# Optimization experiments

Measured on AMD Instinct MI355X. Metric: run time of the kernel, lower is better.

## Reference

```python
import jax, jax.numpy as jnp
import numpy as np

N = 50000   # nodes
E = 600000  # edges (avg degree 12)
D = 128     # node_feat_size == graph_feat_size


def setup_inputs() -> dict:
    key = jax.random.key(0)
    ks = jax.random.split(key, 10)
    return {
        "node_feats": jax.random.normal(ks[0], (N, D), jnp.float32),
        "src": jax.random.randint(ks[1], (E,), 0, N),
        "dst": jax.random.randint(ks[2], (E,), 0, N),
        # project_edge: Linear(2D, 1)
        "W_edge": jax.random.normal(ks[3], (2 * D, 1), jnp.float32) * 0.05,
        "b_edge": jnp.zeros((1,), jnp.float32),
        # project_node: Linear(D, D)
        "W_proj": jax.random.normal(ks[4], (D, D), jnp.float32) * 0.05,
        "b_proj": jnp.zeros((D,), jnp.float32),
        # GRUCell(input=D, hidden=D)
        "W_ih": jax.random.normal(ks[5], (3 * D, D), jnp.float32) * 0.05,
        "W_hh": jax.random.normal(ks[6], (3 * D, D), jnp.float32) * 0.05,
        "b_ih": jnp.zeros((3 * D,), jnp.float32),
        "b_hh": jnp.zeros((3 * D,), jnp.float32),
        # BatchNorm1d(D) affine params (training-mode batch stats)
        "bn_gamma": jnp.ones((D,), jnp.float32),
        "bn_beta": jnp.zeros((D,), jnp.float32),
    }


def reference(node_feats, src, dst, W_edge, b_edge, W_proj, b_proj,
              W_ih, W_hh, b_ih, b_hh, bn_gamma, bn_beta):
    n_nodes = node_feats.shape[0]
    # apply_edges: he = concat([dst_feats, src_feats])  -> [E, 2D]
    he = jnp.concatenate([node_feats[dst], node_feats[src]], axis=1)
    # project_edge: Linear(2D,1) + LeakyReLU(0.01) -> edge logits [E]
    logits = jax.nn.leaky_relu(he @ W_edge + b_edge, 0.01)[:, 0]
    # DGL edge_softmax: softmax over incoming edges of each dst node
    mx = jax.ops.segment_max(logits, dst, num_segments=n_nodes)
    ex = jnp.exp(logits - mx[dst])
    denom = jax.ops.segment_sum(ex, dst, num_segments=n_nodes)
    a = ex / denom[dst]
    e = a + 1.0  # g.edata['e'] = a + 1
    # project_node (dropout is identity in eval) -> hv [N, D]
    hv = node_feats @ W_proj + b_proj
    # src_mul_edge + sum aggregation: c[v] = sum_{(u->v)} hv[u] * e
    msg = hv[src] * e[:, None]                       # [E, D]
    c = jax.ops.segment_sum(msg, dst, num_segments=n_nodes)
    context = jax.nn.elu(c)
    # GRUCell(context, node_feats)
    gi = context @ W_ih.T + b_ih
    gh = node_feats @ W_hh.T + b_hh
    i_r, i_z, i_n = jnp.split(gi, 3, axis=1)
    h_r, h_z, h_n = jnp.split(gh, 3, axis=1)
    r = jax.nn.sigmoid(i_r + h_r)
    z = jax.nn.sigmoid(i_z + h_z)
    n = jnp.tanh(i_n + r * h_n)
    h = (1.0 - z) * n + z * node_feats
    out = jax.nn.relu(h)
    # BatchNorm1d (training-mode batch statistics, eps=1e-5)
    mean = out.mean(axis=0)
    var = out.var(axis=0)
    return (out - mean) / jnp.sqrt(var + 1e-5) * bn_gamma + bn_beta
```

## Files before the change

kernel.cpp:

```cpp
#include <hip/hip_runtime.h>
#include <math.h>

constexpr int D = 128;
constexpr int BCAP = 4096;

typedef __attribute__((ext_vector_type(8))) short short8;
typedef __attribute__((ext_vector_type(4))) float f32x4;
typedef unsigned short ushort_t;
typedef unsigned int uint_t;

__device__ inline ushort_t f2b(float x) {
    uint_t u = __float_as_uint(x);
    uint_t r = u + 0x7fffu + ((u >> 16) & 1u);
    return (ushort_t)(r >> 16);
}
__device__ inline float b2f(ushort_t b) { return __uint_as_float(((uint_t)b) << 16); }

__device__ inline float sigm(float x) { return 1.f / (1.f + __expf(-x)); }
__device__ inline float tanh_(float x) {
    float t = __expf(-2.f * fabsf(x));
    float y = (1.f - t) / (1.f + t);
    return x >= 0.f ? y : -y;
}

__global__ __launch_bounds__(256) void k_prep_w(
    const float* __restrict__ W_ih, const float* __restrict__ W_hh,
    const float* __restrict__ W_proj,
    ushort_t* __restrict__ Wih16, ushort_t* __restrict__ Whh16,
    ushort_t* __restrict__ WpT16,
    int* __restrict__ gcur, float* __restrict__ bn8, int NBK)
{
    int idx = blockIdx.x * 256 + threadIdx.x;
    if (idx < 49152) {
        Wih16[idx] = f2b(W_ih[idx]);
    } else if (idx < 98304) {
        int i = idx - 49152;
        Whh16[i] = f2b(W_hh[i]);
    } else if (idx < 114688) {
        int t = idx - 98304;
        int j = t >> 7, k = t & 127;
        WpT16[t] = f2b(W_proj[k * 128 + j]);
    } else if (idx < 114688 + 256) {
        int t = idx - 114688;
        if (t < NBK) gcur[t] = t * BCAP;
    } else if (idx < 114688 + 256 + 2048) {
        bn8[idx - 114688 - 256] = 0.f;
    }
}

constexpr int EPT = 16;
__global__ __launch_bounds__(256, 2) void k_hv_part(
    const float* __restrict__ nf, const ushort_t* __restrict__ WpT16,
    const float* __restrict__ b_proj, const float* __restrict__ W_edge,
    ushort_t* __restrict__ nf16, ushort_t* __restrict__ hv16,
    float* __restrict__ s_d, float* __restrict__ s_s,
    const int* __restrict__ src, const int* __restrict__ dst,
    int* __restrict__ gcur, uint_t* __restrict__ pre_rec,
    int N, int NBK, int E, int nb_part)
{
    __shared__ ushort_t plds[16384];

    if ((int)blockIdx.x < nb_part) {
        int* cnt   = (int*)plds;
        int* gbase = cnt + 256;
        int tid = threadIdx.x;
        int base = blockIdx.x * (256 * EPT);
        for (int i = tid; i < NBK; i += 256) cnt[i] = 0;
        __syncthreads();
        uint_t rec[EPT], pw[EPT];
#pragma unroll
        for (int i = 0; i < EPT; ++i) {
            int e = base + i * 256 + tid;
            uint_t r = 0, p = 0xFFFFFFFFu;
            if (e < E) {
                int s = src[e], t = dst[e];
                int b = t >> 8;
                int old = atomicAdd(&cnt[b], 1);
                r = (uint_t)s | ((uint_t)(t & 255) << 16);
                p = ((uint_t)b << 16) | (uint_t)old;
            }
            rec[i] = r; pw[i] = p;
        }
        __syncthreads();
        for (int bkt = tid; bkt < NBK; bkt += 256) {
            int c = cnt[bkt];
            gbase[bkt] = c ? atomicAdd(&gcur[bkt], c) : 0;
        }
        __syncthreads();
#pragma unroll
        for (int i = 0; i < EPT; ++i) {
            if (pw[i] != 0xFFFFFFFFu) {
                int b = pw[i] >> 16;
                int old = pw[i] & 0xFFFF;
                pre_rec[gbase[b] + old] = rec[i];
            }
        }
        return;
    }

    int bid = blockIdx.x - nb_part;
    int w = threadIdx.x >> 6, lane = threadIdx.x & 63;
    int am = lane & 15, hi = lane >> 4, ak = hi * 8;

#pragma unroll
    for (int i = 0; i < 8; ++i) {
        int dl = (w * 8 + i) * 4 + hi;
        short8 v = *(const short8*)(WpT16 + (size_t)dl * 128 + am * 8);
        *(short8*)(plds + dl * 128 + ((am ^ (dl & 15)) * 8)) = v;
    }

    int r0 = bid * 64 + w * 16;
    int arow = r0 + am;
    bool aok = arow < N;
    short8 A[4];
    float pd = 0.f, ps = 0.f;
#pragma unroll
    for (int kf = 0; kf < 4; ++kf) {
        int ko = kf * 32 + ak;
        float4 f0 = {0,0,0,0}, f1 = {0,0,0,0};
        if (aok) {
            f0 = *(const float4*)(nf + (size_t)arow * 128 + ko);
            f1 = *(const float4*)(nf + (size_t)arow * 128 + ko + 4);
        }
        pd += f0.x * W_edge[ko]     + f0.y * W_edge[ko + 1]
            + f0.z * W_edge[ko + 2] + f0.w * W_edge[ko + 3]
            + f1.x * W_edge[ko + 4] + f1.y * W_edge[ko + 5]
            + f1.z * W_edge[ko + 6] + f1.w * W_edge[ko + 7];
        ps += f0.x * W_edge[128+ko]     + f0.y * W_edge[128+ko+1]
            + f0.z * W_edge[128+ko+2]   + f0.w * W_edge[128+ko+3]
            + f1.x * W_edge[128+ko+4]   + f1.y * W_edge[128+ko+5]
            + f1.z * W_edge[128+ko+6]   + f1.w * W_edge[128+ko+7];
        short8 a;
        a[0] = (short)f2b(f0.x); a[1] = (short)f2b(f0.y);
        a[2] = (short)f2b(f0.z); a[3] = (short)f2b(f0.w);
        a[4] = (short)f2b(f1.x); a[5] = (short)f2b(f1.y);
        a[6] = (short)f2b(f1.z); a[7] = (short)f2b(f1.w);
        A[kf] = a;
        if (aok) *(short8*)(nf16 + (size_t)arow * 128 + ko) = a;
    }
    pd += __shfl_xor(pd, 16); pd += __shfl_xor(pd, 32);
    ps += __shfl_xor(ps, 16); ps += __shfl_xor(ps, 32);
    if (hi == 0 && aok) { s_d[arow] = pd; s_s[arow] = ps; }

    __syncthreads();

    int crow0 = r0 + hi * 4;
#pragma unroll 2
    for (int nc = 0; nc < 8; ++nc) {
        f32x4 acc = {0.f, 0.f, 0.f, 0.f};
        int col = nc * 16 + am;
#pragma unroll
        for (int kf = 0; kf < 4; ++kf) {
            short8 B = *(const short8*)(plds + col * 128 + (((kf * 4 + hi) ^ am) * 8));
            acc = __builtin_amdgcn_mfma_f32_16x16x32_bf16(A[kf], B, acc, 0, 0, 0);
        }
        float b = b_proj[col];
#pragma unroll
        for (int r = 0; r < 4; ++r) {
            int grow = crow0 + r;
            if (grow < N) hv16[(size_t)grow * 128 + col] = f2b(acc[r] + b);
        }
    }
}

__global__ __launch_bounds__(256) void k_bucket(
    const uint_t* __restrict__ pre_rec, const int* __restrict__ gcur,
    const float* __restrict__ s_d, const float* __restrict__ s_s,
    const float* __restrict__ b_edge,
    int* __restrict__ row_start, int* __restrict__ row_cnt,
    uint2* __restrict__ edge_rec, float* __restrict__ den, int N)
{
    __shared__ int cnt[256], offx[256], cur[256], sdata[256];
    __shared__ float sdl[256], denl[256];
    int b = blockIdx.x, tid = threadIdx.x;
    int node = (b << 8) + tid;
    cnt[tid] = 0; cur[tid] = 0; denl[tid] = 0.f;
    sdl[tid] = (node < N) ? s_d[node] : 0.f;
    __syncthreads();
    int rs0 = b * BCAP, rs1 = gcur[b];
    for (int i = rs0 + tid; i < rs1; i += 256)
        atomicAdd(&cnt[(pre_rec[i] >> 16) & 255], 1);
    __syncthreads();
    int v = cnt[tid];
    int incl = v;
    sdata[tid] = incl; __syncthreads();
#pragma unroll
    for (int off = 1; off < 256; off <<= 1) {
        int add = (tid >= off) ? sdata[tid - off] : 0;
        __syncthreads();
        incl += add;
        sdata[tid] = incl;
        __syncthreads();
    }
    offx[tid] = incl - v;
    if (node < N) {
        row_start[node] = rs0 + incl - v;
        row_cnt[node] = v;
    }
    __syncthreads();
    float bias = b_edge[0];
    for (int i = rs0 + tid; i < rs1; i += 256) {
        uint_t rec = pre_rec[i];
        int sidx = rec & 0xFFFF;
        int dl = (rec >> 16) & 255;
        float l = sdl[dl] + s_s[sidx] + bias;
        l = l > 0.f ? l : 0.01f * l;
        float ev = __expf(l);
        int lp = atomicAdd(&cur[dl], 1);
        uint2 r;
        r.x = (uint_t)sidx;
        r.y = __float_as_uint(ev);
        edge_rec[rs0 + offx[dl] + lp] = r;
        atomicAdd(&denl[dl], ev);
    }
    __syncthreads();
    if (node < N) den[node] = denl[tid];
}

__global__ __launch_bounds__(256) void k_agg4(
    const ushort_t* __restrict__ hv16, const int* __restrict__ row_start,
    const int* __restrict__ row_cnt, const float* __restrict__ den,
    const uint2* __restrict__ edge_rec, ushort_t* __restrict__ ctx16, int N)
{
    __shared__ uint2 elds[8][128];
    int w = threadIdx.x >> 6, lane = threadIdx.x & 63;
    int half = lane >> 5;
    int hl = lane & 31;
    int nid = w * 2 + half;
    int v = blockIdx.x * 8 + nid;
    bool vok = v < N;

    int beg = 0, cnt = 0;
    float dv = 0.f;
    if (vok) {
        beg = row_start[v];
        cnt = row_cnt[v];
        dv = den[v];
        int cap0 = min(cnt, 128);
        for (int c = hl; c < cap0; c += 32)
            elds[nid][c] = edge_rec[beg + c];
    }
    float inv = dv > 0.f ? 1.f / dv : 0.f;

    float c0 = 0.f, c1 = 0.f, c2 = 0.f, c3 = 0.f;
    int cap = min(cnt, 128);
    for (int t0 = 0; t0 < cap; t0 += 8) {
        uint2 p[8];
        float wt[8];
#pragma unroll
        for (int k = 0; k < 8; ++k) {
            int tt = t0 + k;
            uint2 er = elds[nid][tt < cap ? tt : 0];
            wt[k] = (tt < cap) ? fmaf(__uint_as_float(er.y), inv, 1.0f) : 0.f;
            p[k] = ((const uint2*)(hv16 + ((size_t)er.x << 7)))[hl];
        }
#pragma unroll
        for (int k = 0; k < 8; ++k) {
            c0 = fmaf(b2f((ushort_t)p[k].x), wt[k], c0);
            c1 = fmaf(b2f((ushort_t)(p[k].x >> 16)), wt[k], c1);
            c2 = fmaf(b2f((ushort_t)p[k].y), wt[k], c2);
            c3 = fmaf(b2f((ushort_t)(p[k].y >> 16)), wt[k], c3);
        }
    }
    for (int c = 128; c < cnt; ++c) {
        uint2 er = edge_rec[beg + c];
        float wt2 = fmaf(__uint_as_float(er.y), inv, 1.0f);
        uint2 p2 = ((const uint2*)(hv16 + ((size_t)er.x << 7)))[hl];
        c0 = fmaf(b2f((ushort_t)p2.x), wt2, c0);
        c1 = fmaf(b2f((ushort_t)(p2.x >> 16)), wt2, c1);
        c2 = fmaf(b2f((ushort_t)p2.y), wt2, c2);
        c3 = fmaf(b2f((ushort_t)(p2.y >> 16)), wt2, c3);
    }
    if (!vok) return;
    c0 = c0 > 0.f ? c0 : expm1f(c0);
    c1 = c1 > 0.f ? c1 : expm1f(c1);
    c2 = c2 > 0.f ? c2 : expm1f(c2);
    c3 = c3 > 0.f ? c3 : expm1f(c3);
    uint2 outp;
    outp.x = (uint_t)f2b(c0) | ((uint_t)f2b(c1) << 16);
    outp.y = (uint_t)f2b(c2) | ((uint_t)f2b(c3) << 16);
    ((uint2*)ctx16)[(size_t)v * 32 + hl] = outp;
}

__global__ __launch_bounds__(1024, 1) void k_gru_mfma(
    const ushort_t* __restrict__ ctx16, const ushort_t* __restrict__ nf16,
    const ushort_t* __restrict__ Wih16, const ushort_t* __restrict__ Whh16,
    const float* __restrict__ b_ih, const float* __restrict__ b_hh,
    float* __restrict__ out, float* __restrict__ bn8, int N)
{
    __shared__ ushort_t wlds[6 * 8192];
    __shared__ float bnsum[2][16][64];
    int tid = threadIdx.x;
    int w = tid >> 6, lane = tid & 63;
    int am = lane & 15, hi = lane >> 4, ak = hi * 8;
    int g64 = blockIdx.y * 64;

    for (int q = tid; q < 6144; q += 1024) {
        int m = q >> 10;
        int rem = q & 1023;
        int col = rem >> 4;
        int kc = rem & 15;
        const ushort_t* sb = (m & 1) ? Whh16 : Wih16;
        short8 v = *(const short8*)(sb + (size_t)((m >> 1) * 128 + g64 + col) * 128 + kc * 8);
        *(short8*)(wlds + m * 8192 + col * 128 + ((kc ^ (col & 15)) * 8)) = v;
    }
    __syncthreads();

    float br_[4], bz_[4], bi_[4], bh_[4];
#pragma unroll
    for (int cf = 0; cf < 4; ++cf) {
        int dgl = g64 + cf * 16 + am;
        br_[cf] = b_ih[dgl] + b_hh[dgl];
        bz_[cf] = b_ih[128 + dgl] + b_hh[128 + dgl];
        bi_[cf] = b_ih[256 + dgl];
        bh_[cf] = b_hh[256 + dgl];
    }
    float cs[4] = {0,0,0,0}, cs2[4] = {0,0,0,0};

    for (int r0 = blockIdx.x * 256; r0 < N; r0 += gridDim.x * 256) {
        int rbase = r0 + w * 16;
        int arow = rbase + am;
        bool aok = arow < N;
        short8 z8 = {0,0,0,0,0,0,0,0};
        short8 Ac[4], An[4];
#pragma unroll
        for (int kf = 0; kf < 4; ++kf) {
            size_t off = (size_t)arow * 128 + kf * 32 + ak;
            Ac[kf] = aok ? *(const short8*)(ctx16 + off) : z8;
            An[kf] = aok ? *(const short8*)(nf16 + off) : z8;
        }
        int crow0 = rbase + hi * 4;
#pragma unroll 1
        for (int cf = 0; cf < 4; ++cf) {
            int dgl = g64 + cf * 16 + am;
            float hp_pre[4];
#pragma unroll
            for (int r = 0; r < 4; ++r) {
                int grow = crow0 + r;
                hp_pre[r] = (grow < N) ? b2f(nf16[(size_t)grow * 128 + dgl]) : 0.f;
            }
            f32x4 racc = {0,0,0,0}, zacc = {0,0,0,0};
            f32x4 iacc = {0,0,0,0}, hacc = {0,0,0,0};
#pragma unroll
            for (int kf = 0; kf < 4; ++kf) {
                const ushort_t* bp = wlds + (cf * 16 + am) * 128
                                   + ((((kf << 2) + hi) ^ am) * 8);
                short8 Br = *(const short8*)(bp + 0 * 8192);
                short8 Cr = *(const short8*)(bp + 1 * 8192);
                short8 Bz = *(const short8*)(bp + 2 * 8192);
                short8 Cz = *(const short8*)(bp + 3 * 8192);
                short8 Bi = *(const short8*)(bp + 4 * 8192);
                short8 Ch = *(const short8*)(bp + 5 * 8192);
                racc = __builtin_amdgcn_mfma_f32_16x16x32_bf16(Ac[kf], Br, racc, 0, 0, 0);
                racc = __builtin_amdgcn_mfma_f32_16x16x32_bf16(An[kf], Cr, racc, 0, 0, 0);
                zacc = __builtin_amdgcn_mfma_f32_16x16x32_bf16(Ac[kf], Bz, zacc, 0, 0, 0);
                zacc = __builtin_amdgcn_mfma_f32_16x16x32_bf16(An[kf], Cz, zacc, 0, 0, 0);
                iacc = __builtin_amdgcn_mfma_f32_16x16x32_bf16(Ac[kf], Bi, iacc, 0, 0, 0);
                hacc = __builtin_amdgcn_mfma_f32_16x16x32_bf16(An[kf], Ch, hacc, 0, 0, 0);
            }
#pragma unroll
            for (int r = 0; r < 4; ++r) {
                int grow = crow0 + r;
                float rv = sigm(racc[r] + br_[cf]);
                float zv = sigm(zacc[r] + bz_[cf]);
                float nv = tanh_(iacc[r] + bi_[cf] + rv * (hacc[r] + bh_[cf]));
                float h = (1.f - zv) * nv + zv * hp_pre[r];
                h = fmaxf(h, 0.f);
                if (grow < N) out[(size_t)grow * 128 + dgl] = h;
                else h = 0.f;
                cs[cf] += h;
                cs2[cf] = fmaf(h, h, cs2[cf]);
            }
        }
    }

#pragma unroll
    for (int cf = 0; cf < 4; ++cf) {
        cs[cf]  += __shfl_xor(cs[cf], 16);  cs[cf]  += __shfl_xor(cs[cf], 32);
        cs2[cf] += __shfl_xor(cs2[cf], 16); cs2[cf] += __shfl_xor(cs2[cf], 32);
        if (hi == 0) {
            bnsum[0][w][cf * 16 + am] = cs[cf];
            bnsum[1][w][cf * 16 + am] = cs2[cf];
        }
    }
    __syncthreads();
    int bin = (blockIdx.x & 7) * 256;
    if (tid < 64) {
        float s = 0.f;
#pragma unroll
        for (int wv = 0; wv < 16; ++wv) s += bnsum[0][wv][tid];
        atomicAdd(&bn8[bin + g64 + tid], s);
    } else if (tid < 128) {
        int c2 = tid - 64;
        float s2 = 0.f;
#pragma unroll
        for (int wv = 0; wv < 16; ++wv) s2 += bnsum[1][wv][c2];
        atomicAdd(&bn8[bin + 128 + g64 + c2], s2);
    }
}

__global__ __launch_bounds__(256) void k_bnnorm(
    float* __restrict__ out, const float* __restrict__ bn8,
    const float* __restrict__ gamma, const float* __restrict__ beta, int N)
{
    __shared__ float a_s[128], c_s[128];
    int tid = threadIdx.x;
    if (tid < 128) {
        float s = 0.f, s2 = 0.f;
#pragma unroll
        for (int b = 0; b < 8; ++b) {
            s  += bn8[b * 256 + tid];
            s2 += bn8[b * 256 + 128 + tid];
        }
        float invN = 1.f / (float)N;
        float mean = s * invN;
        float var = s2 * invN - mean * mean;
        float a = rsqrtf(var + 1e-5f) * gamma[tid];
        a_s[tid] = a;
        c_s[tid] = beta[tid] - mean * a;
    }
    __syncthreads();
    int idx = blockIdx.x * 256 + tid;
    int total = N * 32;
    if (idx >= total) return;
    float4 x = ((const float4*)out)[idx];
    int d0 = (idx * 4) & 127;
    x.x = x.x * a_s[d0]     + c_s[d0];
    x.y = x.y * a_s[d0 + 1] + c_s[d0 + 1];
    x.z = x.z * a_s[d0 + 2] + c_s[d0 + 2];
    x.w = x.w * a_s[d0 + 3] + c_s[d0 + 3];
    ((float4*)out)[idx] = x;
}

extern "C" void kernel_launch(void* const* d_in, const int* in_sizes, int n_in,
                              void* d_out, int out_size, void* d_ws, size_t ws_size,
                              hipStream_t stream)
{
    const float* nf     = (const float*)d_in[0];
    const int*   src    = (const int*)  d_in[1];
    const int*   dst    = (const int*)  d_in[2];
    const float* W_edge = (const float*)d_in[3];
    const float* b_edge = (const float*)d_in[4];
    const float* W_proj = (const float*)d_in[5];
    const float* b_proj = (const float*)d_in[6];
    const float* W_ih   = (const float*)d_in[7];
    const float* W_hh   = (const float*)d_in[8];
    const float* b_ih   = (const float*)d_in[9];
    const float* b_hh   = (const float*)d_in[10];
    const float* bn_g   = (const float*)d_in[11];
    const float* bn_b   = (const float*)d_in[12];

    const int N   = in_sizes[0] / D;
    const int E   = in_sizes[1];
    const int NBK = (N + 255) >> 8;

    float* ws = (float*)d_ws;
    float* s_d        = ws;
    float* s_s        = ws + (size_t)N;
    float* den        = ws + (size_t)2 * N;
    int*   row_start  = (int*)(ws + (size_t)3 * N);
    int*   row_cnt    = (int*)(ws + (size_t)4 * N);
    int*   gcur       = (int*)(ws + (size_t)5 * N);
    float* bn8        = ws + (size_t)5 * N + 256;
    uint_t* pre_rec   = (uint_t*)(ws + (size_t)5 * N + 2304);
    uint2*  edge_rec  = (uint2*)(pre_rec + (size_t)NBK * BCAP);
    ushort_t* nf16    = (ushort_t*)(edge_rec + (size_t)NBK * BCAP);
    ushort_t* hv16    = nf16 + (size_t)N * 128;
    ushort_t* ctx16   = hv16 + (size_t)N * 128;
    ushort_t* Wih16   = ctx16 + (size_t)N * 128;
    ushort_t* Whh16   = Wih16 + 384 * 128;
    ushort_t* WpT16   = Whh16 + 384 * 128;

    float* outp = (float*)d_out;

    int nb_part = (E + 256 * EPT - 1) / (256 * EPT);
    int nb_hv   = (N + 63) / 64;

    k_prep_w<<<(114688 + 2304 + 255) / 256, 256, 0, stream>>>(
        W_ih, W_hh, W_proj, Wih16, Whh16, WpT16, gcur, bn8, NBK);
    k_hv_part<<<nb_part + nb_hv, 256, 0, stream>>>(
        nf, WpT16, b_proj, W_edge, nf16, hv16, s_d, s_s,
        src, dst, gcur, pre_rec, N, NBK, E, nb_part);
    k_bucket<<<NBK, 256, 0, stream>>>(pre_rec, gcur, s_d, s_s, b_edge,
                                      row_start, row_cnt, edge_rec, den, N);
    k_agg4<<<(N + 7) / 8, 256, 0, stream>>>(hv16, row_start, row_cnt, den,
                                            edge_rec, ctx16, N);
    k_gru_mfma<<<dim3(128, 2), 1024, 0, stream>>>(ctx16, nf16, Wih16, Whh16,
                                                  b_ih, b_hh, outp, bn8, N);
    k_bnnorm<<<(N * 32 + 255) / 256, 256, 0, stream>>>(outp, bn8, bn_g, bn_b, N);
}
```

Before: 120.2 us.

## Fuse GRU and BatchNorm via cooperative grid sync, keeping outputs in registers

After: 153.1 us. +27.4%, slower.

```diff
diff --git a/kernel.cpp b/kernel.cpp
--- a/kernel.cpp
+++ b/kernel.cpp
@@ -1,5 +1,8 @@
 #include <hip/hip_runtime.h>
+#include <hip/hip_cooperative_groups.h>
 #include <math.h>
+
+namespace cg = cooperative_groups;
 
 constexpr int D = 128;
 constexpr int BCAP = 4096;
@@ -282,14 +285,16 @@
     ((uint2*)ctx16)[(size_t)v * 32 + hl] = outp;
 }
 
-__global__ __launch_bounds__(1024, 1) void k_gru_mfma(
+__global__ __launch_bounds__(1024, 1) void k_gru_bn(
     const ushort_t* __restrict__ ctx16, const ushort_t* __restrict__ nf16,
     const ushort_t* __restrict__ Wih16, const ushort_t* __restrict__ Whh16,
     const float* __restrict__ b_ih, const float* __restrict__ b_hh,
-    float* __restrict__ out, float* __restrict__ bn8, int N)
+    float* __restrict__ out, float* __restrict__ bn8,
+    const float* __restrict__ gamma, const float* __restrict__ beta, int N)
 {
     __shared__ ushort_t wlds[6 * 8192];
     __shared__ float bnsum[2][16][64];
+    __shared__ float a_s[64], c_s[64];
     int tid = threadIdx.x;
     int w = tid >> 6, lane = tid & 63;
     int am = lane & 15, hi = lane >> 4, ak = hi * 8;
@@ -316,8 +321,12 @@
         bh_[cf] = b_hh[256 + dgl];
     }
     float cs[4] = {0,0,0,0}, cs2[4] = {0,0,0,0};
-
-    for (int r0 = blockIdx.x * 256; r0 < N; r0 += gridDim.x * 256) {
+    float hreg[2][4][4];
+
+#pragma unroll
+    for (int g = 0; g < 2; ++g) {
+        int r0 = blockIdx.x * 256 + g * 32768;
+        if (r0 >= N) continue;
         int rbase = r0 + w * 16;
         int arow = rbase + am;
         bool aok = arow < N;
@@ -366,8 +375,8 @@
                 float nv = tanh_(iacc[r] + bi_[cf] + rv * (hacc[r] + bh_[cf]));
                 float h = (1.f - zv) * nv + zv * hp_pre[r];
                 h = fmaxf(h, 0.f);
-                if (grow < N) out[(size_t)grow * 128 + dgl] = h;
-                else h = 0.f;
+                if (grow >= N) h = 0.f;
+                hreg[g][cf][r] = h;
                 cs[cf] += h;
                 cs2[cf] = fmaf(h, h, cs2[cf]);
             }
@@ -397,39 +406,44 @@
         for (int wv = 0; wv < 16; ++wv) s2 += bnsum[1][wv][c2];
         atomicAdd(&bn8[bin + 128 + g64 + c2], s2);
     }
-}
-
-__global__ __launch_bounds__(256) void k_bnnorm(
-    float* __restrict__ out, const float* __restrict__ bn8,
-    const float* __restrict__ gamma, const float* __restrict__ beta, int N)
-{
-    __shared__ float a_s[128], c_s[128];
-    int tid = threadIdx.x;
-    if (tid < 128) {
+
+    cg::this_grid().sync();
+
+    if (tid < 64) {
+        int gc = g64 + tid;
         float s = 0.f, s2 = 0.f;
 #pragma unroll
         for (int b = 0; b < 8; ++b) {
-            s  += bn8[b * 256 + tid];
-            s2 += bn8[b * 256 + 128 + tid];
+            s  += bn8[b * 256 + gc];
+            s2 += bn8[b * 256 + 128 + gc];
         }
         float invN = 1.f / (float)N;
         float mean = s * invN;
         float var = s2 * invN - mean * mean;
-        float a = rsqrtf(var + 1e-5f) * gamma[tid];
+        float a = rsqrtf(var + 1e-5f) * gamma[gc];
         a_s[tid] = a;
-        c_s[tid] = beta[tid] - mean * a;
-    }
-    __syncthreads();
-    int idx = blockIdx.x * 256 + tid;
-    int total = N * 32;
-    if (idx >= total) return;
-    float4 x = ((const float4*)out)[idx];
-    int d0 = (idx * 4) & 127;
-    x.x = x.x * a_s[d0]     + c_s[d0];
-    x.y = x.y * a_s[d0 + 1] + c_s[d0 + 1];
-    x.z = x.z * a_s[d0 + 2] + c_s[d0 + 2];
-    x.w = x.w * a_s[d0 + 3] + c_s[d0 + 3];
-    ((float4*)out)[idx] = x;
+        c_s[tid] = beta[gc] - mean * a;
+    }
+    __syncthreads();
+
+#pragma unroll
+    for (int g = 0; g < 2; ++g) {
+        int r0 = blockIdx.x * 256 + g * 32768;
+        if (r0 >= N) continue;
+        int crow0 = r0 + w * 16 + hi * 4;
+#pragma unroll
+        for (int cf = 0; cf < 4; ++cf) {
+            int lc = cf * 16 + am;
+            int dgl = g64 + lc;
+            float a = a_s[lc], c = c_s[lc];
+#pragma unroll
+            for (int r = 0; r < 4; ++r) {
+                int grow = crow0 + r;
+                if (grow < N)
+                    out[(size_t)grow * 128 + dgl] = hreg[g][cf][r] * a + c;
+            }
+        }
+    }
 }
 
 extern "C" void kernel_launch(void* const* d_in, const int* in_sizes, int n_in,
@@ -485,7 +499,14 @@
                                       row_start, row_cnt, edge_rec, den, N);
     k_agg4<<<(N + 7) / 8, 256, 0, stream>>>(hv16, row_start, row_cnt, den,
                                             edge_rec, ctx16, N);
-    k_gru_mfma<<<dim3(128, 2), 1024, 0, stream>>>(ctx16, nf16, Wih16, Whh16,
-                                                  b_ih, b_hh, outp, bn8, N);
-    k_bnnorm<<<(N * 32 + 255) / 256, 256, 0, stream>>>(outp, bn8, bn_g, bn_b, N);
-}
+    {
+        int Nv = N;
+        void* args[] = {
+            (void*)&ctx16, (void*)&nf16, (void*)&Wih16, (void*)&Whh16,
+            (void*)&b_ih, (void*)&b_hh, (void*)&outp, (void*)&bn8,
+            (void*)&bn_g, (void*)&bn_b, (void*)&Nv
+        };
+        hipLaunchCooperativeKernel((const void*)k_gru_bn, dim3(128, 2),
+                                   dim3(1024), args, 0, stream);
+    }
+}
```
